# Kernel tuning notes

Measured on AMD Instinct MI355X. Metric: run time of the kernel, lower is better.

Reference implementation:

```python
import jax, jax.numpy as jnp
import numpy as np

NUM_HEADS = 4
LOCAL_RADIUS = 2


def setup_inputs() -> dict:
    key = jax.random.key(0)
    ks = jax.random.split(key, 7)
    B, C, H, W = 1, 256, 40, 40
    O = 256  # out_channels
    s = 1.0 / np.sqrt(C).astype(np.float32)
    x = jax.random.normal(ks[0], (B, C, H, W), dtype=jnp.float32)
    Wq = jax.random.normal(ks[1], (C, O), dtype=jnp.float32) * s
    Wk = jax.random.normal(ks[2], (C, O), dtype=jnp.float32) * s
    Wv = jax.random.normal(ks[3], (C, O), dtype=jnp.float32) * s
    bq = jnp.zeros((O,), jnp.float32)
    bk = jnp.zeros((O,), jnp.float32)
    bv = jnp.zeros((O,), jnp.float32)
    return {"x": x, "Wq": Wq, "bq": bq, "Wk": Wk, "bk": bk, "Wv": Wv, "bv": bv}


def reference(x, Wq, bq, Wk, bk, Wv, bv):
    B, C, H, W = x.shape
    N = H * W
    O = Wq.shape[1]
    hd = O // NUM_HEADS
    # Faithful to torch: x.view(B, N, -1) is a raw row-major reshape of (B,C,H,W)
    xf = x.reshape(B, N, C)
    # projections -> (B, heads, N, head_dim)
    q = (xf @ Wq + bq).reshape(B, N, NUM_HEADS, hd).transpose(0, 2, 1, 3)
    k = (xf @ Wk + bk).reshape(B, N, NUM_HEADS, hd).transpose(0, 2, 1, 3)
    v = (xf @ Wv + bv).reshape(B, N, NUM_HEADS, hd).transpose(0, 2, 1, 3)
    scale = jnp.asarray(O, jnp.float32) ** 0.5
    acc = jnp.zeros_like(v)
    # 25 shifted full-attention passes; roll is over (heads, points) axes,
    # exactly matching torch key.roll(shifts=(h,w), dims=(-3,-2)).
    for h in range(-LOCAL_RADIUS, LOCAL_RADIUS + 1):
        for w in range(-LOCAL_RADIUS, LOCAL_RADIUS + 1):
            rk = jnp.roll(k, shift=(h, w), axis=(1, 2))
            scores = jnp.einsum('bhnd,bhmd->bhnm', q, rk) / scale  # (B,h,N,N)
            attn = jax.nn.softmax(scores, axis=-1)
            rv = jnp.roll(v, shift=(-h, -w), axis=(1, 2))
            acc = acc + jnp.einsum('bhnm,bhmd->bhnd', attn, rv)
    # (B, heads, N, hd) -> (B, N, O)
    return acc.transpose(0, 2, 1, 3).reshape(B, N, O)
```

## Files before the change

### kernel.cpp

```cpp
#include <hip/hip_runtime.h>
#include <hip/hip_bf16.h>
#include <stdint.h>

typedef __attribute__((ext_vector_type(8))) __bf16 bf16x8;
typedef __attribute__((ext_vector_type(4))) float f32x4;

#define N_PTS 1600
#define HD    64

#define OFF_XC   0u
#define OFF_WT   819200u
#define OFF_BIAS 1212416u
#define OFF_VHT  1213952u
#define OFF_QH   2033152u
#define OFF_KH   2852352u
#define OFF_KF   0u
#define OFF_OP   2852352u
#define OFF_LP   9405952u
#define OFF_VF   9610752u

__device__ __forceinline__ float bf2f(ushort h) {
  union { uint32_t u; float f; } v; v.u = ((uint32_t)h) << 16; return v.f;
}
__device__ __forceinline__ ushort f2bf(float f) {
  union { float f; uint32_t u; } v; v.f = f;
  uint32_t u = v.u;
  return (ushort)((u + 0x7FFFu + ((u >> 16) & 1u)) >> 16);
}
__device__ __forceinline__ uint32_t pk2(float a, float b) {
  union { __hip_bfloat162 h; uint32_t u; } cv;
  cv.h = __float22bfloat162_rn(make_float2(a, b));
  return cv.u;
}

__device__ __forceinline__ int detect_f32(const ushort* xu, int* shflag) {
  int t = threadIdx.x & 255;
  if (t == 0) *shflag = 0;
  __syncthreads();
  int local = 0;
#pragma unroll
  for (int i = 0; i < 4; ++i) {
    float v = bf2f(xu[(t * 4 + i) * 2]);
    if (!(fabsf(v) < 1e4f)) local = 1;
  }
  if (local) atomicOr(shflag, 1);
  __syncthreads();
  return *shflag;
}

__global__ void k_prep(const void* __restrict__ x, const void* __restrict__ Wq,
                       const void* __restrict__ bq, const void* __restrict__ Wk,
                       const void* __restrict__ bk, const void* __restrict__ Wv,
                       const void* __restrict__ bv, char* __restrict__ ws) {
  __shared__ int shflag;
  __shared__ ushort tileb[32][33];
  int isf32 = detect_f32((const ushort*)x, &shflag);
  int b = blockIdx.x, t = threadIdx.x;

  if (b < 400) {
    ushort4 o;
    if (isf32) {
      float4 f = ((const float4*)x)[b * 256 + t];
      o.x = f2bf(f.x); o.y = f2bf(f.y); o.z = f2bf(f.z); o.w = f2bf(f.w);
    } else {
      o = ((const ushort4*)x)[b * 256 + t];
    }
    ((ushort4*)(ws + OFF_XC))[b * 256 + t] = o;
  } else if (b < 592) {
    int w = b - 400, z = w >> 6, tile = w & 63;
    const void* W = (z == 0) ? Wq : ((z == 1) ? Wk : Wv);
    int o0 = (tile & 7) * 32, k0 = (tile >> 3) * 32;
    int tx = t & 31, ty = t >> 5;
#pragma unroll
    for (int i = 0; i < 32; i += 8) {
      int kk = (k0 + ty + i) * 256 + o0 + tx;
      tileb[ty + i][tx] = isf32 ? f2bf(((const float*)W)[kk]) : ((const ushort*)W)[kk];
    }
    __syncthreads();
    ushort* WT = (ushort*)(ws + OFF_WT) + z * 65536;
#pragma unroll
    for (int i = 0; i < 32; i += 8)
      WT[(o0 + ty + i) * 256 + k0 + tx] = tileb[tx][ty + i];
  } else {
    ushort* bb = (ushort*)(ws + OFF_BIAS);
#pragma unroll
    for (int z = 0; z < 3; ++z) {
      const void* B = (z == 0) ? bq : ((z == 1) ? bk : bv);
      bb[z * 256 + t] = isf32 ? f2bf(((const float*)B)[t]) : ((const ushort*)B)[t];
    }
  }
}

__launch_bounds__(256)
__global__ void k_proj(const ushort* __restrict__ X, const ushort* __restrict__ WT,
                       const ushort* __restrict__ bias3,
                       ushort* __restrict__ Qh, ushort* __restrict__ Kh, ushort* __restrict__ VhT) {
  int z = blockIdx.z;
  const ushort* WTz = WT + z * 65536;
  const ushort* bias = bias3 + z * 256;
  int n0 = blockIdx.x * 16;
  int head = threadIdx.x >> 6;
  int lane = threadIdx.x & 63;
  int c = lane & 15, quad = lane >> 4;

  f32x4 acc[4];
#pragma unroll
  for (int i = 0; i < 4; ++i) acc[i] = (f32x4){0.f, 0.f, 0.f, 0.f};

  const ushort* xrow = X + (n0 + c) * 256;
#pragma unroll
  for (int kt = 0; kt < 8; ++kt) {
    bf16x8 a = *(const bf16x8*)(xrow + kt * 32 + quad * 8);
#pragma unroll
    for (int os = 0; os < 4; ++os) {
      bf16x8 bfr = *(const bf16x8*)(WTz + (head * 64 + os * 16 + c) * 256 + kt * 32 + quad * 8);
      acc[os] = __builtin_amdgcn_mfma_f32_16x16x32_bf16(a, bfr, acc[os], 0, 0, 0);
    }
  }
  if (z == 2) {
#pragma unroll
    for (int os = 0; os < 4; ++os) {
      float bval = bf2f(bias[head * 64 + os * 16 + c]);
      ushort4 v;
      v.x = f2bf(acc[os][0] + bval); v.y = f2bf(acc[os][1] + bval);
      v.z = f2bf(acc[os][2] + bval); v.w = f2bf(acc[os][3] + bval);
      *(ushort4*)(VhT + (head * 64 + os * 16 + c) * N_PTS + n0 + quad * 4) = v;
    }
  } else {
    float scale = (z == 0) ? 0.0625f * 1.44269504088896f : 1.0f;
    ushort* out = (z == 0) ? Qh : Kh;
#pragma unroll
    for (int os = 0; os < 4; ++os) {
      float bval = bf2f(bias[head * 64 + os * 16 + c]);
#pragma unroll
      for (int r = 0; r < 4; ++r)
        out[head * (N_PTS * HD) + (n0 + quad * 4 + r) * HD + os * 16 + c] =
            f2bf((acc[os][r] + bval) * scale);
    }
  }
}

__global__ void k_frag(const ushort* __restrict__ Kh, const ushort* __restrict__ VhT,
                       ushort* __restrict__ Kf, ushort* __restrict__ Vf) {
  int q = blockIdx.x * 256 + threadIdx.x;
  int isV = q >= 51200;
  int idx = isV ? q - 51200 : q;
  int lane = idx & 63, ch = (idx >> 6) & 3;
  int rest = idx >> 8;
  int t = rest % 50, g = rest / 50;
  int c = lane & 15, quad = lane >> 4;
  if (!isV) {
    int perm = ((c >> 2) << 3) + (c & 3);
    int key = t * 32 + perm + ((ch >> 1) << 2);
    int d0 = (ch & 1) * 32 + quad * 8;
    bf16x8 v = *(const bf16x8*)(Kh + (size_t)(g * N_PTS + key) * HD + d0);
    *(bf16x8*)(Kf + (size_t)idx * 8) = v;
  } else {
    int d = ch * 16 + c;
    int m0 = t * 32 + quad * 8;
    const ushort* row = VhT + (size_t)(g * HD + d) * N_PTS;
    int mp = (m0 == 0) ? 1592 : m0 - 8;
    int mn = (m0 == 1592) ? 0 : m0 + 8;
    union { bf16x8 v[3]; ushort us[24]; } w;
    w.v[0] = *(const bf16x8*)(row + mp);
    w.v[1] = *(const bf16x8*)(row + m0);
    w.v[2] = *(const bf16x8*)(row + mn);
    union { ushort us[8]; bf16x8 v; } o;
#pragma unroll
    for (int j = 0; j < 8; ++j) {
      float s = bf2f(w.us[4 + j]) + bf2f(w.us[6 + j]) + bf2f(w.us[8 + j]) +
                bf2f(w.us[10 + j]) + bf2f(w.us[12 + j]);
      o.us[j] = f2bf(s);
    }
    *(bf16x8*)(Vf + (size_t)idx * 8) = o.v;
  }
}

__device__ __forceinline__ bf16x8 pack_p8(const f32x4& s0, const f32x4& s1, float& lp) {
  float e0 = exp2f(s0[0]), e1 = exp2f(s0[1]), e2 = exp2f(s0[2]), e3 = exp2f(s0[3]);
  float e4 = exp2f(s1[0]), e5 = exp2f(s1[1]), e6 = exp2f(s1[2]), e7 = exp2f(s1[3]);
  lp += ((e0 + e1) + (e2 + e3)) + ((e4 + e5) + (e6 + e7));
  union { uint32_t u[4]; bf16x8 v; } r;
  r.u[0] = pk2(e0, e1); r.u[1] = pk2(e2, e3);
  r.u[2] = pk2(e4, e5); r.u[3] = pk2(e6, e7);
  return r.v;
}

__launch_bounds__(256, 4)
__global__ void k_attn(const ushort* __restrict__ Qh, const ushort* __restrict__ Kf,
                       const ushort* __restrict__ Vf, ushort* __restrict__ Opart,
                       float* __restrict__ Lpart) {
  int qt = blockIdx.x;
  int yy = blockIdx.y;
  int z  = blockIdx.z;
  int hp = yy >> 2, kg = yy & 3;
  int vg = (2 * hp - kg + 8) & 3;
  int tid = threadIdx.x, sp = tid >> 6, lane = tid & 63;
  int c = lane & 15, quad = lane >> 4;
  int n0 = qt * 16;

  __shared__ float obuf[4][16][68];
  __shared__ float lbuf[4][16];

  const ushort* q0row = Qh + ((hp    ) * N_PTS + n0 + c) * HD;
  const ushort* q1row = Qh + ((hp + 2) * N_PTS + n0 + c) * HD;
  bf16x8 qa00 = *(const bf16x8*)(q0row + quad * 8);
  bf16x8 qa01 = *(const bf16x8*)(q0row + 32 + quad * 8);
  bf16x8 qa10 = *(const bf16x8*)(q1row + quad * 8);
  bf16x8 qa11 = *(const bf16x8*)(q1row + 32 + quad * 8);

  f32x4 oacc0[4], oacc1[4];
#pragma unroll
  for (int i = 0; i < 4; ++i) {
    oacc0[i] = (f32x4){0.f, 0.f, 0.f, 0.f};
    oacc1[i] = (f32x4){0.f, 0.f, 0.f, 0.f};
  }
  float lp0 = 0.f, lp1 = 0.f;

  int off = (sp == 0) ? 0 : (sp == 1) ? 7 : (sp == 2) ? 13 : 19;
  int iters = (sp == 0) ? 7 : 6;
  int t0 = z * 25 + off;
  const f32x4 z4 = (f32x4){0.f, 0.f, 0.f, 0.f};

  const char* kfp = (const char*)Kf + (size_t)(kg * 50 + t0) * 4096 + lane * 16;
  const char* vfp = (const char*)Vf + (size_t)(vg * 50 + t0) * 4096 + lane * 16;

  for (int it = 0; it < iters; ++it) {
    const char* kt = kfp + it * 4096;
    const char* vt = vfp + it * 4096;
    bf16x8 ka0 = *(const bf16x8*)(kt);
    bf16x8 ka1 = *(const bf16x8*)(kt + 1024);
    bf16x8 kb0 = *(const bf16x8*)(kt + 2048);
    bf16x8 kb1 = *(const bf16x8*)(kt + 3072);
    bf16x8 vb[4];
#pragma unroll
    for (int ds = 0; ds < 4; ++ds)
      vb[ds] = *(const bf16x8*)(vt + ds * 1024);

    f32x4 s0 = __builtin_amdgcn_mfma_f32_16x16x32_bf16(ka0, qa00, z4, 0, 0, 0);
    s0 = __builtin_amdgcn_mfma_f32_16x16x32_bf16(ka1, qa01, s0, 0, 0, 0);
    f32x4 s1 = __builtin_amdgcn_mfma_f32_16x16x32_bf16(kb0, qa00, z4, 0, 0, 0);
    s1 = __builtin_amdgcn_mfma_f32_16x16x32_bf16(kb1, qa01, s1, 0, 0, 0);
    bf16x8 pa = pack_p8(s0, s1, lp0);
#pragma unroll
    for (int ds = 0; ds < 4; ++ds)
      oacc0[ds] = __builtin_amdgcn_mfma_f32_16x16x32_bf16(pa, vb[ds], oacc0[ds], 0, 0, 0);

    s0 = __builtin_amdgcn_mfma_f32_16x16x32_bf16(ka0, qa10, z4, 0, 0, 0);
    s0 = __builtin_amdgcn_mfma_f32_16x16x32_bf16(ka1, qa11, s0, 0, 0, 0);
    s1 = __builtin_amdgcn_mfma_f32_16x16x32_bf16(kb0, qa10, z4, 0, 0, 0);
    s1 = __builtin_amdgcn_mfma_f32_16x16x32_bf16(kb1, qa11, s1, 0, 0, 0);
    bf16x8 pa1 = pack_p8(s0, s1, lp1);
#pragma unroll
    for (int ds = 0; ds < 4; ++ds)
      oacc1[ds] = __builtin_amdgcn_mfma_f32_16x16x32_bf16(pa1, vb[ds], oacc1[ds], 0, 0, 0);
  }

  lp0 += __shfl_xor(lp0, 16, 64); lp0 += __shfl_xor(lp0, 32, 64);
  lp1 += __shfl_xor(lp1, 16, 64); lp1 += __shfl_xor(lp1, 32, 64);

#pragma unroll
  for (int h = 0; h < 2; ++h) {
    __syncthreads();
    const f32x4* oa = h ? oacc1 : oacc0;
#pragma unroll
    for (int ds = 0; ds < 4; ++ds)
#pragma unroll
      for (int r = 0; r < 4; ++r)
        obuf[sp][quad * 4 + r][ds * 16 + c] = oa[ds][r];
    if (quad == 0) lbuf[sp][c] = h ? lp1 : lp0;
    __syncthreads();

    int q = tid >> 4, d0 = (tid & 15) * 4;
    f32x4 a = *(const f32x4*)&obuf[0][q][d0];
    a += *(const f32x4*)&obuf[1][q][d0];
    a += *(const f32x4*)&obuf[2][q][d0];
    a += *(const f32x4*)&obuf[3][q][d0];
    float l = lbuf[0][q] + lbuf[1][q] + lbuf[2][q] + lbuf[3][q];
    int hq = hp + 2 * h;
    union { uint32_t u[2]; } wv;
    wv.u[0] = pk2(a[0], a[1]);
    wv.u[1] = pk2(a[2], a[3]);
    *(uint2*)&Opart[(size_t)((z * 4 + kg) * N_PTS + n0 + q) * 256 + hq * 64 + d0] =
        *(uint2*)wv.u;
    if ((tid & 15) == 0)
      Lpart[((z * 4 + kg) * 4 + hq) * N_PTS + n0 + q] = l;
  }
}

__global__ void k_out(const ushort* __restrict__ Opart, const float* __restrict__ Lpart,
                      const void* __restrict__ x, void* __restrict__ out) {
  __shared__ int shflag;
  int isf32 = detect_f32((const ushort*)x, &shflag);
  int idx = blockIdx.x * 256 + threadIdx.x;
  int n = idx >> 8, o = idx & 255, hq = o >> 6;
  float acc = 0.f;
#pragma unroll
  for (int kg = 0; kg < 4; ++kg) {
    float num = bf2f(Opart[(size_t)((0 + kg) * N_PTS + n) * 256 + o]) +
                bf2f(Opart[(size_t)((4 + kg) * N_PTS + n) * 256 + o]);
    float l = Lpart[((0 + kg) * 4 + hq) * N_PTS + n] +
              Lpart[((4 + kg) * 4 + hq) * N_PTS + n];
    float w = (kg == ((hq + 2) & 3)) ? 2.f : 1.f;
    acc += w * num / l;
  }
  if (isf32) ((float*)out)[idx] = acc;
  else       ((ushort*)out)[idx] = f2bf(acc);
}

extern "C" void kernel_launch(void* const* d_in, const int* in_sizes, int n_in,
                              void* d_out, int out_size, void* d_ws, size_t ws_size,
                              hipStream_t stream) {
  char* ws = (char*)d_ws;
  ushort* Xc    = (ushort*)(ws + OFF_XC);
  ushort* WT    = (ushort*)(ws + OFF_WT);
  ushort* bias3 = (ushort*)(ws + OFF_BIAS);
  ushort* VhT   = (ushort*)(ws + OFF_VHT);
  ushort* Qh    = (ushort*)(ws + OFF_QH);
  ushort* Kh    = (ushort*)(ws + OFF_KH);
  ushort* Kf    = (ushort*)(ws + OFF_KF);
  ushort* Vf    = (ushort*)(ws + OFF_VF);
  ushort* Opart = (ushort*)(ws + OFF_OP);
  float*  Lpart = (float*)(ws + OFF_LP);

  k_prep<<<593, 256, 0, stream>>>(d_in[0], d_in[1], d_in[2], d_in[3],
                                  d_in[4], d_in[5], d_in[6], ws);
  k_proj<<<dim3(100, 1, 3), 256, 0, stream>>>(Xc, WT, bias3, Qh, Kh, VhT);
  k_frag<<<400, 256, 0, stream>>>(Kh, VhT, Kf, Vf);
  k_attn<<<dim3(100, 8, 2), 256, 0, stream>>>(Qh, Kf, Vf, Opart, Lpart);
  k_out<<<1600, 256, 0, stream>>>(Opart, Lpart, d_in[0], d_out);
}
```

Measured before the change: 112.4 us.

## Process two 16-query subtiles per attention block to reuse K/V fragments

Each attention block now handles 32 queries instead of 16, so every K and V fragment loaded from global memory feeds twice as many MFMA ops. This halves the grid and the total K/V traffic. The grid is also reordered so head/key-group blocks for the same query tile sit next to each other. The cost is roughly double the accumulator registers and LDS per block, so occupancy drops (launch bounds go from 4 to 2) and there are fewer blocks to hide latency.

```diff
diff --git a/kernel.cpp b/kernel.cpp
--- a/kernel.cpp
+++ b/kernel.cpp
@@ -186,41 +186,56 @@
   return r.v;
 }
 
-__launch_bounds__(256, 4)
+__device__ __forceinline__ bf16x8 qk_p(const bf16x8& ka0, const bf16x8& ka1,
+                                       const bf16x8& kb0, const bf16x8& kb1,
+                                       const bf16x8& qa0, const bf16x8& qa1, float& lp) {
+  const f32x4 z4 = (f32x4){0.f, 0.f, 0.f, 0.f};
+  f32x4 s0 = __builtin_amdgcn_mfma_f32_16x16x32_bf16(ka0, qa0, z4, 0, 0, 0);
+  s0 = __builtin_amdgcn_mfma_f32_16x16x32_bf16(ka1, qa1, s0, 0, 0, 0);
+  f32x4 s1 = __builtin_amdgcn_mfma_f32_16x16x32_bf16(kb0, qa0, z4, 0, 0, 0);
+  s1 = __builtin_amdgcn_mfma_f32_16x16x32_bf16(kb1, qa1, s1, 0, 0, 0);
+  return pack_p8(s0, s1, lp);
+}
+
+__launch_bounds__(256, 2)
 __global__ void k_attn(const ushort* __restrict__ Qh, const ushort* __restrict__ Kf,
                        const ushort* __restrict__ Vf, ushort* __restrict__ Opart,
                        float* __restrict__ Lpart) {
-  int qt = blockIdx.x;
-  int yy = blockIdx.y;
+  int yy = blockIdx.x;
+  int qt2 = blockIdx.y;
   int z  = blockIdx.z;
   int hp = yy >> 2, kg = yy & 3;
   int vg = (2 * hp - kg + 8) & 3;
   int tid = threadIdx.x, sp = tid >> 6, lane = tid & 63;
   int c = lane & 15, quad = lane >> 4;
-  int n0 = qt * 16;
-
-  __shared__ float obuf[4][16][68];
-  __shared__ float lbuf[4][16];
-
-  const ushort* q0row = Qh + ((hp    ) * N_PTS + n0 + c) * HD;
-  const ushort* q1row = Qh + ((hp + 2) * N_PTS + n0 + c) * HD;
-  bf16x8 qa00 = *(const bf16x8*)(q0row + quad * 8);
-  bf16x8 qa01 = *(const bf16x8*)(q0row + 32 + quad * 8);
-  bf16x8 qa10 = *(const bf16x8*)(q1row + quad * 8);
-  bf16x8 qa11 = *(const bf16x8*)(q1row + 32 + quad * 8);
-
-  f32x4 oacc0[4], oacc1[4];
-#pragma unroll
-  for (int i = 0; i < 4; ++i) {
-    oacc0[i] = (f32x4){0.f, 0.f, 0.f, 0.f};
-    oacc1[i] = (f32x4){0.f, 0.f, 0.f, 0.f};
-  }
-  float lp0 = 0.f, lp1 = 0.f;
+  int n0 = qt2 * 32;
+
+  __shared__ float obuf[4][32][68];
+  __shared__ float lbuf[4][32];
+
+  bf16x8 qa[2][2][2];
+#pragma unroll
+  for (int qs = 0; qs < 2; ++qs)
+#pragma unroll
+    for (int h = 0; h < 2; ++h) {
+      const ushort* qrow = Qh + ((hp + 2 * h) * N_PTS + n0 + qs * 16 + c) * HD;
+      qa[qs][h][0] = *(const bf16x8*)(qrow + quad * 8);
+      qa[qs][h][1] = *(const bf16x8*)(qrow + 32 + quad * 8);
+    }
+
+  f32x4 oacc[2][2][4];
+  float lp[2][2] = {{0.f, 0.f}, {0.f, 0.f}};
+#pragma unroll
+  for (int qs = 0; qs < 2; ++qs)
+#pragma unroll
+    for (int h = 0; h < 2; ++h)
+#pragma unroll
+      for (int i = 0; i < 4; ++i)
+        oacc[qs][h][i] = (f32x4){0.f, 0.f, 0.f, 0.f};
 
   int off = (sp == 0) ? 0 : (sp == 1) ? 7 : (sp == 2) ? 13 : 19;
   int iters = (sp == 0) ? 7 : 6;
   int t0 = z * 25 + off;
-  const f32x4 z4 = (f32x4){0.f, 0.f, 0.f, 0.f};
 
   const char* kfp = (const char*)Kf + (size_t)(kg * 50 + t0) * 4096 + lane * 16;
   const char* vfp = (const char*)Vf + (size_t)(vg * 50 + t0) * 4096 + lane * 16;
@@ -237,53 +252,58 @@
     for (int ds = 0; ds < 4; ++ds)
       vb[ds] = *(const bf16x8*)(vt + ds * 1024);
 
-    f32x4 s0 = __builtin_amdgcn_mfma_f32_16x16x32_bf16(ka0, qa00, z4, 0, 0, 0);
-    s0 = __builtin_amdgcn_mfma_f32_16x16x32_bf16(ka1, qa01, s0, 0, 0, 0);
-    f32x4 s1 = __builtin_amdgcn_mfma_f32_16x16x32_bf16(kb0, qa00, z4, 0, 0, 0);
-    s1 = __builtin_amdgcn_mfma_f32_16x16x32_bf16(kb1, qa01, s1, 0, 0, 0);
-    bf16x8 pa = pack_p8(s0, s1, lp0);
-#pragma unroll
-    for (int ds = 0; ds < 4; ++ds)
-      oacc0[ds] = __builtin_amdgcn_mfma_f32_16x16x32_bf16(pa, vb[ds], oacc0[ds], 0, 0, 0);
-
-    s0 = __builtin_amdgcn_mfma_f32_16x16x32_bf16(ka0, qa10, z4, 0, 0, 0);
-    s0 = __builtin_amdgcn_mfma_f32_16x16x32_bf16(ka1, qa11, s0, 0, 0, 0);
-    s1 = __builtin_amdgcn_mfma_f32_16x16x32_bf16(kb0, qa10, z4, 0, 0, 0);
-    s1 = __builtin_amdgcn_mfma_f32_16x16x32_bf16(kb1, qa11, s1, 0, 0, 0);
-    bf16x8 pa1 = pack_p8(s0, s1, lp1);
-#pragma unroll
-    for (int ds = 0; ds < 4; ++ds)
-      oacc1[ds] = __builtin_amdgcn_mfma_f32_16x16x32_bf16(pa1, vb[ds], oacc1[ds], 0, 0, 0);
-  }
-
-  lp0 += __shfl_xor(lp0, 16, 64); lp0 += __shfl_xor(lp0, 32, 64);
-  lp1 += __shfl_xor(lp1, 16, 64); lp1 += __shfl_xor(lp1, 32, 64);
+#pragma unroll
+    for (int qs = 0; qs < 2; ++qs)
+#pragma unroll
+      for (int h = 0; h < 2; ++h) {
+        bf16x8 pa = qk_p(ka0, ka1, kb0, kb1, qa[qs][h][0], qa[qs][h][1], lp[qs][h]);
+#pragma unroll
+        for (int ds = 0; ds < 4; ++ds)
+          oacc[qs][h][ds] =
+              __builtin_amdgcn_mfma_f32_16x16x32_bf16(pa, vb[ds], oacc[qs][h][ds], 0, 0, 0);
+      }
+  }
+
+#pragma unroll
+  for (int qs = 0; qs < 2; ++qs)
+#pragma unroll
+    for (int h = 0; h < 2; ++h) {
+      float l = lp[qs][h];
+      l += __shfl_xor(l, 16, 64); l += __shfl_xor(l, 32, 64);
+      lp[qs][h] = l;
+    }
 
 #pragma unroll
   for (int h = 0; h < 2; ++h) {
     __syncthreads();
-    const f32x4* oa = h ? oacc1 : oacc0;
-#pragma unroll
-    for (int ds = 0; ds < 4; ++ds)
-#pragma unroll
-      for (int r = 0; r < 4; ++r)
-        obuf[sp][quad * 4 + r][ds * 16 + c] = oa[ds][r];
-    if (quad == 0) lbuf[sp][c] = h ? lp1 : lp0;
+#pragma unroll
+    for (int qs = 0; qs < 2; ++qs) {
+#pragma unroll
+      for (int ds = 0; ds < 4; ++ds)
+#pragma unroll
+        for (int r = 0; r < 4; ++r)
+          obuf[sp][qs * 16 + quad * 4 + r][ds * 16 + c] = oacc[qs][h][ds][r];
+      if (quad == 0) lbuf[sp][qs * 16 + c] = lp[qs][h];
+    }
     __syncthreads();
 
-    int q = tid >> 4, d0 = (tid & 15) * 4;
-    f32x4 a = *(const f32x4*)&obuf[0][q][d0];
-    a += *(const f32x4*)&obuf[1][q][d0];
-    a += *(const f32x4*)&obuf[2][q][d0];
-    a += *(const f32x4*)&obuf[3][q][d0];
-    float l = lbuf[0][q] + lbuf[1][q] + lbuf[2][q] + lbuf[3][q];
+    int q = tid >> 3, d0 = (tid & 7) * 8;
+    f32x4 a0 = (f32x4){0.f, 0.f, 0.f, 0.f};
+    f32x4 a1 = (f32x4){0.f, 0.f, 0.f, 0.f};
+    float l = 0.f;
+#pragma unroll
+    for (int sp2 = 0; sp2 < 4; ++sp2) {
+      a0 += *(const f32x4*)&obuf[sp2][q][d0];
+      a1 += *(const f32x4*)&obuf[sp2][q][d0 + 4];
+      l += lbuf[sp2][q];
+    }
     int hq = hp + 2 * h;
-    union { uint32_t u[2]; } wv;
-    wv.u[0] = pk2(a[0], a[1]);
-    wv.u[1] = pk2(a[2], a[3]);
-    *(uint2*)&Opart[(size_t)((z * 4 + kg) * N_PTS + n0 + q) * 256 + hq * 64 + d0] =
-        *(uint2*)wv.u;
-    if ((tid & 15) == 0)
+    union { uint32_t u[4]; } wv;
+    wv.u[0] = pk2(a0[0], a0[1]); wv.u[1] = pk2(a0[2], a0[3]);
+    wv.u[2] = pk2(a1[0], a1[1]); wv.u[3] = pk2(a1[2], a1[3]);
+    *(uint4*)&Opart[(size_t)((z * 4 + kg) * N_PTS + n0 + q) * 256 + hq * 64 + d0] =
+        *(uint4*)wv.u;
+    if ((tid & 7) == 0)
       Lpart[((z * 4 + kg) * 4 + hq) * N_PTS + n0 + q] = l;
   }
 }
@@ -327,6 +347,6 @@
                                   d_in[4], d_in[5], d_in[6], ws);
   k_proj<<<dim3(100, 1, 3), 256, 0, stream>>>(Xc, WT, bias3, Qh, Kh, VhT);
   k_frag<<<400, 256, 0, stream>>>(Kh, VhT, Kf, Vf);
-  k_attn<<<dim3(100, 8, 2), 256, 0, stream>>>(Qh, Kf, Vf, Opart, Lpart);
+  k_attn<<<dim3(8, 50, 2), 256, 0, stream>>>(Qh, Kf, Vf, Opart, Lpart);
   k_out<<<1600, 256, 0, stream>>>(Opart, Lpart, d_in[0], d_out);
 }
```

After: 117.6 us. 1.05x slower.
